# Kernel tuning notes

Measured on AMD Instinct MI355X. Metric: run time of the kernel, lower is better.

## Reference

```python
import jax, jax.numpy as jnp
import numpy as np

B, C, H, W = 16, 64, 64, 64
O, BR, K = 128, 3, 3  # out_channels, branch, kernel


def setup_inputs() -> dict:
    key = jax.random.key(0)
    k1, k2, k3, k4 = jax.random.split(key, 4)
    x = jax.random.normal(k1, (B, C, H, W), dtype=jnp.float32)
    w1 = jax.random.normal(k2, (O, BR * BR), dtype=jnp.float32) * 0.1
    w2 = jax.random.normal(k3, (O, BR), dtype=jnp.float32) * 0.1
    conn = jax.random.randint(k4, (O * BR * BR,), 0, C * K * K)
    return {"x": x, "w1": w1, "w2": w2, "conn": conn}


def reference(x, w1, w2, conn):
    # replicate pad (kernel 3x3, extra_pad=0 -> pad 1 on each side)
    x_pad = jnp.pad(x, ((0, 0), (0, 0), (1, 1), (1, 1)), mode='edge')
    # extract 3x3 patches, stride 1; loop is over fixed 9 kernel offsets
    # patches: [B, C, H, W, K*K] with (i,j) row-major, matching torch unfold
    patches = jnp.stack(
        [x_pad[:, :, i:i + H, j:j + W] for i in range(K) for j in range(K)],
        axis=-1,
    )
    # -> [B, H, W, C*K*K]   (flatten order C, k0, k1 as in the torch reshape)
    patches = jnp.transpose(patches, (0, 2, 3, 1, 4)).reshape(B, H, W, C * K * K)
    # random gather along the unfolded axis -> [B, H, W, O, BR*BR]
    g = patches[..., conn].reshape(B, H, W, O, BR * BR)
    g = jnp.transpose(g, (0, 3, 1, 2, 4))  # [B, O, H, W, BR*BR]
    d = jnp.abs(g - w1[:, None, None, :])  # broadcast w1 [O,1,1,BR*BR]
    ma = jnp.max(d.reshape(B, O, H, W, BR, BR), axis=-1)  # amax over inner branch
    mi = jnp.min(jnp.abs(ma - w2[:, None, None, :]), axis=-1)  # amin over branch
    return mi  # [B, O, H, W]
```

## Files before the change

### kernel.cpp

```cpp
#include <hip/hip_runtime.h>

#define BB 16
#define CC 64
#define HH 64
#define WW 64
#define OO 128

__device__ __forceinline__ float dpp_shr1(float src, float edge) {
    int old = __builtin_bit_cast(int, edge);
    int s   = __builtin_bit_cast(int, src);
    int r = __builtin_amdgcn_update_dpp(old, s, 0x111, 0xF, 0xF, false);
    return __builtin_bit_cast(float, r);
}
__device__ __forceinline__ float dpp_shl1(float src, float edge) {
    int old = __builtin_bit_cast(int, edge);
    int s   = __builtin_bit_cast(int, src);
    int r = __builtin_amdgcn_update_dpp(old, s, 0x101, 0xF, 0xF, false);
    return __builtin_bit_cast(float, r);
}

__global__ __launch_bounds__(256) void minimax_conv_kernel(
    const float* __restrict__ x, const float* __restrict__ w1,
    const float* __restrict__ w2, const int* __restrict__ conn,
    float* __restrict__ out)
{
    const int tid  = threadIdx.x;
    const int L    = tid & 15;
    const int hrow = tid >> 4;
    const int bid = blockIdx.x;
    const int ochunk = bid >> 6;
    const int region = bid & 63;
    const int b  = region >> 2;
    const int h0 = (region & 3) * 16;
    const int h  = h0 + hrow;

    int rowoff[3];
    #pragma unroll
    for (int i = 0; i < 3; ++i) {
        int r = h + i - 1;
        r = r < 0 ? 0 : (r > HH - 1 ? HH - 1 : r);
        rowoff[i] = r * WW + 4 * L;
    }

    const float* xb = x + (size_t)b * (CC * HH * WW);

    #pragma unroll
    for (int oi = 0; oi < 4; ++oi) {
        const int o = ochunk * 4 + oi;

        float res0, res1, res2, res3;
        #pragma unroll
        for (int p = 0; p < 3; ++p) {
            float e0, e1, e2, e3;
            #pragma unroll
            for (int tt = 0; tt < 3; ++tt) {
                const int t = p * 3 + tt;
                const int v = conn[o * 9 + t];
                const int c = v / 9;
                const int r = v - c * 9;
                const int i = r / 3;
                const int j = r - i * 3;
                const float w1v = w1[o * 9 + t];

                const float4 q = *(const float4*)(xb + (size_t)c * (HH * WW) + rowoff[i]);

                float v0, v1, v2, v3;
                if (j == 0) {
                    const float le = dpp_shr1(q.w, q.x);
                    v0 = le;  v1 = q.x; v2 = q.y; v3 = q.z;
                } else if (j == 1) {
                    v0 = q.x; v1 = q.y; v2 = q.z; v3 = q.w;
                } else {
                    const float re = dpp_shl1(q.x, q.w);
                    v0 = q.y; v1 = q.z; v2 = q.w; v3 = re;
                }
                const float d0 = fabsf(v0 - w1v);
                const float d1 = fabsf(v1 - w1v);
                const float d2 = fabsf(v2 - w1v);
                const float d3 = fabsf(v3 - w1v);
                if (tt == 0) { e0 = d0; e1 = d1; e2 = d2; e3 = d3; }
                else {
                    e0 = fmaxf(e0, d0); e1 = fmaxf(e1, d1);
                    e2 = fmaxf(e2, d2); e3 = fmaxf(e3, d3);
                }
            }
            const float w2v = w2[o * 3 + p];
            const float m0 = fabsf(e0 - w2v);
            const float m1 = fabsf(e1 - w2v);
            const float m2 = fabsf(e2 - w2v);
            const float m3 = fabsf(e3 - w2v);
            if (p == 0) { res0 = m0; res1 = m1; res2 = m2; res3 = m3; }
            else {
                res0 = fminf(res0, m0); res1 = fminf(res1, m1);
                res2 = fminf(res2, m2); res3 = fminf(res3, m3);
            }
        }

        float4 outv; outv.x = res0; outv.y = res1; outv.z = res2; outv.w = res3;
        *(float4*)(out + ((((size_t)b * OO + o) * HH + h) * WW + 4 * L)) = outv;
    }
}

extern "C" void kernel_launch(void* const* d_in, const int* in_sizes, int n_in,
                              void* d_out, int out_size, void* d_ws, size_t ws_size,
                              hipStream_t stream) {
    const float* x    = (const float*)d_in[0];
    const float* w1   = (const float*)d_in[1];
    const float* w2   = (const float*)d_in[2];
    const int*   conn = (const int*)d_in[3];
    float* out = (float*)d_out;

    const int blocks = 32 * 64;
    minimax_conv_kernel<<<blocks, 256, 0, stream>>>(x, w1, w2, conn, out);
}
```

Before: 29.80 us.

## Stage input row tile with halo in LDS and compute all output channels per block

Each block now copies a 4-row tile of the input, plus a one-row halo on each side and all 64 channels, into 96 KB of shared memory. It then computes all 128 output channels for those rows, with each of the 8 waves handling 16 channels. This replaces the scattered per-output-channel global gathers of input rows with cheap LDS reads and reuses the staged tile across every output channel. In exchange the grid shrinks to 256 large blocks at one block per CU, which means low occupancy. The load phase is also not overlapped with compute, and halo rows are loaded redundantly.

```diff
diff --git a/kernel.cpp b/kernel.cpp
--- a/kernel.cpp
+++ b/kernel.cpp
@@ -5,6 +5,8 @@
 #define HH 64
 #define WW 64
 #define OO 128
+#define HALO 6
+#define LDS_BYTES (CC * HALO * WW * 4)
 
 __device__ __forceinline__ float dpp_shr1(float src, float edge) {
     int old = __builtin_bit_cast(int, edge);
@@ -19,34 +21,46 @@
     return __builtin_bit_cast(float, r);
 }
 
-__global__ __launch_bounds__(256) void minimax_conv_kernel(
+extern "C" __global__ __launch_bounds__(512, 1) void minimax_conv_kernel(
     const float* __restrict__ x, const float* __restrict__ w1,
     const float* __restrict__ w2, const int* __restrict__ conn,
     float* __restrict__ out)
 {
-    const int tid  = threadIdx.x;
-    const int L    = tid & 15;
-    const int hrow = tid >> 4;
+    extern __shared__ float xs[];
+
+    const int tid = threadIdx.x;
     const int bid = blockIdx.x;
-    const int ochunk = bid >> 6;
-    const int region = bid & 63;
-    const int b  = region >> 2;
-    const int h0 = (region & 3) * 16;
-    const int h  = h0 + hrow;
-
-    int rowoff[3];
-    #pragma unroll
-    for (int i = 0; i < 3; ++i) {
-        int r = h + i - 1;
-        r = r < 0 ? 0 : (r > HH - 1 ? HH - 1 : r);
-        rowoff[i] = r * WW + 4 * L;
-    }
+    const int b  = bid >> 4;
+    const int r0 = (bid & 15) * 4;
 
     const float* xb = x + (size_t)b * (CC * HH * WW);
 
     #pragma unroll
-    for (int oi = 0; oi < 4; ++oi) {
-        const int o = ochunk * 4 + oi;
+    for (int rnd = 0; rnd < 12; ++rnd) {
+        const int f   = rnd * 512 + tid;
+        const int c   = f / 96;
+        const int rem = f * 4 - c * (HALO * WW);
+        const int rl  = rem >> 6;
+        const int col = rem & 63;
+        int rimg = r0 - 1 + rl;
+        rimg = rimg < 0 ? 0 : (rimg > HH - 1 ? HH - 1 : rimg);
+        const float4 v = *(const float4*)(xb + (c * HH + rimg) * WW + col);
+        *(float4*)(xs + f * 4) = v;
+    }
+    __syncthreads();
+
+    const int lane = tid & 63;
+    const int row  = lane >> 4;
+    const int L    = lane & 15;
+    const int osub = __builtin_amdgcn_readfirstlane(tid >> 6);
+
+    const int ro0 = (row + 0) * WW + 4 * L;
+    const int ro1 = (row + 1) * WW + 4 * L;
+    const int ro2 = (row + 2) * WW + 4 * L;
+
+    #pragma unroll 2
+    for (int oo = 0; oo < 16; ++oo) {
+        const int o = oo * 8 + osub;
 
         float res0, res1, res2, res3;
         #pragma unroll
@@ -57,12 +71,13 @@
                 const int t = p * 3 + tt;
                 const int v = conn[o * 9 + t];
                 const int c = v / 9;
-                const int r = v - c * 9;
-                const int i = r / 3;
-                const int j = r - i * 3;
+                const int rr = v - c * 9;
+                const int i = rr / 3;
+                const int j = rr - i * 3;
                 const float w1v = w1[o * 9 + t];
 
-                const float4 q = *(const float4*)(xb + (size_t)c * (HH * WW) + rowoff[i]);
+                const int ro = (i == 0) ? ro0 : ((i == 1) ? ro1 : ro2);
+                const float4 q = *(const float4*)(xs + c * (HALO * WW) + ro);
 
                 float v0, v1, v2, v3;
                 if (j == 0) {
@@ -97,7 +112,7 @@
         }
 
         float4 outv; outv.x = res0; outv.y = res1; outv.z = res2; outv.w = res3;
-        *(float4*)(out + ((((size_t)b * OO + o) * HH + h) * WW + 4 * L)) = outv;
+        *(float4*)(out + (((size_t)b * OO + o) * HH + (r0 + row)) * WW + 4 * L) = outv;
     }
 }
 
@@ -110,6 +125,9 @@
     const int*   conn = (const int*)d_in[3];
     float* out = (float*)d_out;
 
-    const int blocks = 32 * 64;
-    minimax_conv_kernel<<<blocks, 256, 0, stream>>>(x, w1, w2, conn, out);
+    hipFuncSetAttribute((const void*)minimax_conv_kernel,
+                        hipFuncAttributeMaxDynamicSharedMemorySize, LDS_BYTES);
+
+    const int blocks = BB * 16;
+    minimax_conv_kernel<<<blocks, 512, LDS_BYTES, stream>>>(x, w1, w2, conn, out);
 }
```

Measured after the change: 42.22 us. +41.7%, slower.

## Double-buffer tap loads across output channels and use nontemporal stores

Applied to the files above, without the earlier changes.

Restructures the per-thread loop over four output channels into a software pipeline: the nine float4 tap loads for two channels are issued up front, and the next channel's loads start while the current one computes. Outputs are written with nontemporal stores, and launch bounds now request four blocks per SM. The aim is to hide gather latency and keep output writes from occupying cache, at the cost of higher register pressure from holding two batches of 9 float4 values.

```diff
diff --git a/kernel.cpp b/kernel.cpp
--- a/kernel.cpp
+++ b/kernel.cpp
@@ -1,10 +1,12 @@
 #include <hip/hip_runtime.h>
 
-#define BB 16
 #define CC 64
 #define HH 64
 #define WW 64
 #define OO 128
+#define HW (HH * WW)
+
+typedef float f32x4 __attribute__((ext_vector_type(4)));
 
 __device__ __forceinline__ float dpp_shr1(float src, float edge) {
     int old = __builtin_bit_cast(int, edge);
@@ -19,7 +21,71 @@
     return __builtin_bit_cast(float, r);
 }
 
-__global__ __launch_bounds__(256) void minimax_conv_kernel(
+struct Batch { float4 q[9]; int j[9]; };
+
+__device__ __forceinline__ void load_taps(Batch& B, const float* __restrict__ xb,
+                                          const int* __restrict__ conn, int o,
+                                          const int ro0, const int ro1, const int ro2) {
+    #pragma unroll
+    for (int t = 0; t < 9; ++t) {
+        const int v  = conn[o * 9 + t];
+        const int c  = v / 9;
+        const int r9 = v - c * 9;
+        const int i  = r9 / 3;
+        B.j[t] = r9 - i * 3;
+        const int ro = (i == 0) ? ro0 : ((i == 1) ? ro1 : ro2);
+        B.q[t] = *(const float4*)(xb + c * HW + ro);
+    }
+}
+
+__device__ __forceinline__ f32x4 compute_o(const Batch& B,
+                                           const float* __restrict__ w1,
+                                           const float* __restrict__ w2, int o) {
+    float r0, r1, r2, r3;
+    #pragma unroll
+    for (int p = 0; p < 3; ++p) {
+        float e0, e1, e2, e3;
+        #pragma unroll
+        for (int tt = 0; tt < 3; ++tt) {
+            const int t = p * 3 + tt;
+            const float w1v = w1[o * 9 + t];
+            const float4 q = B.q[t];
+            float v0, v1, v2, v3;
+            if (B.j[t] == 0) {
+                const float le = dpp_shr1(q.w, q.x);
+                v0 = le;  v1 = q.x; v2 = q.y; v3 = q.z;
+            } else if (B.j[t] == 1) {
+                v0 = q.x; v1 = q.y; v2 = q.z; v3 = q.w;
+            } else {
+                const float re = dpp_shl1(q.x, q.w);
+                v0 = q.y; v1 = q.z; v2 = q.w; v3 = re;
+            }
+            const float d0 = fabsf(v0 - w1v);
+            const float d1 = fabsf(v1 - w1v);
+            const float d2 = fabsf(v2 - w1v);
+            const float d3 = fabsf(v3 - w1v);
+            if (tt == 0) { e0 = d0; e1 = d1; e2 = d2; e3 = d3; }
+            else {
+                e0 = fmaxf(e0, d0); e1 = fmaxf(e1, d1);
+                e2 = fmaxf(e2, d2); e3 = fmaxf(e3, d3);
+            }
+        }
+        const float w2v = w2[o * 3 + p];
+        const float m0 = fabsf(e0 - w2v);
+        const float m1 = fabsf(e1 - w2v);
+        const float m2 = fabsf(e2 - w2v);
+        const float m3 = fabsf(e3 - w2v);
+        if (p == 0) { r0 = m0; r1 = m1; r2 = m2; r3 = m3; }
+        else {
+            r0 = fminf(r0, m0); r1 = fminf(r1, m1);
+            r2 = fminf(r2, m2); r3 = fminf(r3, m3);
+        }
+    }
+    f32x4 res; res.x = r0; res.y = r1; res.z = r2; res.w = r3;
+    return res;
+}
+
+__global__ __launch_bounds__(256, 4) void minimax_conv_kernel(
     const float* __restrict__ x, const float* __restrict__ w1,
     const float* __restrict__ w2, const int* __restrict__ conn,
     float* __restrict__ out)
@@ -34,71 +100,35 @@
     const int h0 = (region & 3) * 16;
     const int h  = h0 + hrow;
 
-    int rowoff[3];
-    #pragma unroll
-    for (int i = 0; i < 3; ++i) {
-        int r = h + i - 1;
-        r = r < 0 ? 0 : (r > HH - 1 ? HH - 1 : r);
-        rowoff[i] = r * WW + 4 * L;
-    }
+    int r0i = h - 1;     r0i = r0i < 0 ? 0 : r0i;
+    int r2i = h + 1;     r2i = r2i > HH - 1 ? HH - 1 : r2i;
+    const int ro0 = r0i * WW + 4 * L;
+    const int ro1 = h   * WW + 4 * L;
+    const int ro2 = r2i * WW + 4 * L;
 
-    const float* xb = x + (size_t)b * (CC * HH * WW);
+    const float* xb = x + (size_t)b * (CC * HW);
+    const int ob = ochunk * 4;
+    float* outb = out + (((size_t)b * OO + ob) * HH + h) * WW + 4 * L;
+    const size_t ostride = (size_t)HW;
 
-    #pragma unroll
-    for (int oi = 0; oi < 4; ++oi) {
-        const int o = ochunk * 4 + oi;
+    Batch B0, B1;
+    load_taps(B0, xb, conn, ob + 0, ro0, ro1, ro2);
+    load_taps(B1, xb, conn, ob + 1, ro0, ro1, ro2);
 
-        float res0, res1, res2, res3;
-        #pragma unroll
-        for (int p = 0; p < 3; ++p) {
-            float e0, e1, e2, e3;
-            #pragma unroll
-            for (int tt = 0; tt < 3; ++tt) {
-                const int t = p * 3 + tt;
-                const int v = conn[o * 9 + t];
-                const int c = v / 9;
-                const int r = v - c * 9;
-                const int i = r / 3;
-                const int j = r - i * 3;
-                const float w1v = w1[o * 9 + t];
+    f32x4 r;
+    r = compute_o(B0, w1, w2, ob + 0);
+    __builtin_nontemporal_store(r, (f32x4*)(outb + 0 * ostride));
+    load_taps(B0, xb, conn, ob + 2, ro0, ro1, ro2);
 
-                const float4 q = *(const float4*)(xb + (size_t)c * (HH * WW) + rowoff[i]);
+    r = compute_o(B1, w1, w2, ob + 1);
+    __builtin_nontemporal_store(r, (f32x4*)(outb + 1 * ostride));
+    load_taps(B1, xb, conn, ob + 3, ro0, ro1, ro2);
 
-                float v0, v1, v2, v3;
-                if (j == 0) {
-                    const float le = dpp_shr1(q.w, q.x);
-                    v0 = le;  v1 = q.x; v2 = q.y; v3 = q.z;
-                } else if (j == 1) {
-                    v0 = q.x; v1 = q.y; v2 = q.z; v3 = q.w;
-                } else {
-                    const float re = dpp_shl1(q.x, q.w);
-                    v0 = q.y; v1 = q.z; v2 = q.w; v3 = re;
-                }
-                const float d0 = fabsf(v0 - w1v);
-                const float d1 = fabsf(v1 - w1v);
-                const float d2 = fabsf(v2 - w1v);
-                const float d3 = fabsf(v3 - w1v);
-                if (tt == 0) { e0 = d0; e1 = d1; e2 = d2; e3 = d3; }
-                else {
-                    e0 = fmaxf(e0, d0); e1 = fmaxf(e1, d1);
-                    e2 = fmaxf(e2, d2); e3 = fmaxf(e3, d3);
-                }
-            }
-            const float w2v = w2[o * 3 + p];
-            const float m0 = fabsf(e0 - w2v);
-            const float m1 = fabsf(e1 - w2v);
-            const float m2 = fabsf(e2 - w2v);
-            const float m3 = fabsf(e3 - w2v);
-            if (p == 0) { res0 = m0; res1 = m1; res2 = m2; res3 = m3; }
-            else {
-                res0 = fminf(res0, m0); res1 = fminf(res1, m1);
-                res2 = fminf(res2, m2); res3 = fminf(res3, m3);
-            }
-        }
+    r = compute_o(B0, w1, w2, ob + 2);
+    __builtin_nontemporal_store(r, (f32x4*)(outb + 2 * ostride));
 
-        float4 outv; outv.x = res0; outv.y = res1; outv.z = res2; outv.w = res3;
-        *(float4*)(out + ((((size_t)b * OO + o) * HH + h) * WW + 4 * L)) = outv;
-    }
+    r = compute_o(B1, w1, w2, ob + 3);
+    __builtin_nontemporal_store(r, (f32x4*)(outb + 3 * ostride));
 }
 
 extern "C" void kernel_launch(void* const* d_in, const int* in_sizes, int n_in,
```

Result: slower. 38.15 us (+28.0%).
